# Optimization experiments

Measured on AMD Instinct MI355X. Metric: run time of the kernel, lower is better.

Reference implementation:

```python
import jax, jax.numpy as jnp
import numpy as np

D_MODEL = 1024
HEADS = 16
SCALE = float(np.sqrt(D_MODEL / HEADS))  # sqrt(d_k) = sqrt(64) = 8


def setup_inputs() -> dict:
    key = jax.random.key(0)
    ks = jax.random.split(key, 5)
    B, S, D = 4, 2048, D_MODEL
    q = jax.random.normal(ks[0], (B, S, D), dtype=jnp.float32)
    init = 0.02
    wq = jax.random.normal(ks[1], (D, D), dtype=jnp.float32) * init
    wk = jax.random.normal(ks[2], (D, D), dtype=jnp.float32) * init
    wv = jax.random.normal(ks[3], (D, D), dtype=jnp.float32) * init
    wo = jax.random.normal(ks[4], (D, D), dtype=jnp.float32) * init
    return {"q": q, "wq": wq, "wk": wk, "wv": wv, "wo": wo}


def reference(q, wq, wk, wv, wo):
    # Faithful to the source: NO head split is ever performed.
    B, S, D = q.shape
    # nn.Linear convention: y = x @ W.T, weight is [out, in]
    Q = jnp.einsum('bsd,ed->bse', q, wq)
    K = jnp.einsum('bsd,ed->bse', q, wk)
    V = jnp.einsum('bsd,ed->bse', q, wv)
    scores = jnp.einsum('bqe,bke->bqk', Q, K) / SCALE  # [B, S, S]
    attn = jax.nn.softmax(scores, axis=-1)
    out = jnp.einsum('bqk,bke->bqe', attn, V)  # [B, S, D]
    # Source bug reproduced: transpose(1,2).contiguous().view(B, S, -1)
    # => reshape the [B, D, S] contiguous buffer back to [B, S, D].
    out = jnp.transpose(out, (0, 2, 1)).reshape(B, S, D)
    return jnp.einsum('bsd,ed->bse', out, wo)
```

## Files before the change

kernel.cpp:

```cpp
#include <hip/hip_runtime.h>
#include <hip/hip_bf16.h>
#include <stdint.h>

typedef __bf16 bf16;
typedef __attribute__((ext_vector_type(8))) __bf16 bf16x8;
typedef __attribute__((ext_vector_type(4))) float f32x4;
typedef __attribute__((ext_vector_type(8))) unsigned short u16x8;

#define LDS_U32 __attribute__((address_space(3))) uint32_t
#define GLB_U32 const __attribute__((address_space(1))) uint32_t
#define GLOAD16(g, l) __builtin_amdgcn_global_load_lds((GLB_U32*)(g), (LDS_U32*)(l), 16, 0, 0)

#define DSR(dst, addr, OFFLIT) \
  asm volatile("ds_read_b128 %0, %1 offset:" OFFLIT : "=v"(dst) : "v"(addr))

#define WAIT_LGKM0() asm volatile("s_waitcnt lgkmcnt(0)")
#define WAIT_LGKM4() asm volatile("s_waitcnt lgkmcnt(4)")
#define WAIT_VMN(n)  asm volatile("s_waitcnt vmcnt(" #n ")")
#define SB()         __builtin_amdgcn_sched_barrier(0)

__global__ __launch_bounds__(256) void cvt_all(const float* __restrict__ q,
                                               const float* __restrict__ wq,
                                               const float* __restrict__ wk,
                                               const float* __restrict__ wv,
                                               const float* __restrict__ wo,
                                               bf16* __restrict__ qb,
                                               bf16* __restrict__ W3,
                                               bf16* __restrict__ wob) {
  const int b = blockIdx.x;
  const float* src;
  bf16* dst;
  int within;
  if (b < 2048) { src = q; dst = qb; within = b; }
  else {
    const int seg = (b - 2048) >> 8;
    within = (b - 2048) & 255;
    if (seg == 0)      { src = wq; dst = W3; }
    else if (seg == 1) { src = wk; dst = W3 + 1048576; }
    else if (seg == 2) { src = wv; dst = W3 + 2097152; }
    else               { src = wo; dst = wob; }
  }
  const int off = within * 1024;
#pragma unroll
  for (int it = 0; it < 4; ++it) {
    const int j = off + it * 256 + threadIdx.x;
    float4 v = reinterpret_cast<const float4*>(src)[j];
    ushort4 o;
    o.x = __builtin_bit_cast(unsigned short, (bf16)v.x);
    o.y = __builtin_bit_cast(unsigned short, (bf16)v.y);
    o.z = __builtin_bit_cast(unsigned short, (bf16)v.z);
    o.w = __builtin_bit_cast(unsigned short, (bf16)v.w);
    reinterpret_cast<ushort4*>(dst)[j] = o;
  }
}

template <int EPI, int WN>
__global__ __launch_bounds__(512, 2) void g256(const bf16* __restrict__ A,
                                               const bf16* __restrict__ Bm,
                                               void* __restrict__ Cp,
                                               int K, float alpha,
                                               long sA, long sB, long sC, int ldc,
                                               int CW, int CH) {
  constexpr int BN = WN * 64;
  constexpr uint32_t PARB = 32768u + WN * 8192u;
  __shared__ bf16 smem_[PARB];
  const long z = blockIdx.z;
  const int t = threadIdx.x;
  const int l = t & 63;
  const int w = t >> 6;
  const int wr = (w >> 2) * 128;
  const int wc = (w & 3) * (WN * 16);
  const int NT = K >> 6;

  int bx, by;
  {
    const int gx = (int)gridDim.x;
    const int gy = (int)gridDim.y;
    const int nxy = gx * gy;
    const int f = (int)blockIdx.y * gx + (int)blockIdx.x;
    const int cgx = (CW > 0) ? gx / CW : 0;
    if ((nxy & 7) == 0 && CW > 0 && CH > 0 && gx % CW == 0 && gy % CH == 0 &&
        cgx * (gy / CH) == 8) {
      const int xcd = f & 7;
      const int i = f >> 3;
      const int cx = xcd % cgx;
      const int cy = xcd / cgx;
      bx = cx * CW + (i % CW);
      by = cy * CH + (i / CW);
    } else if ((nxy & 7) == 0) {
      const int qq = nxy >> 3;
      const int wg = (f & 7) * qq + (f >> 3);
      bx = wg % gx;
      by = wg / gx;
    } else {
      bx = (int)blockIdx.x;
      by = (int)blockIdx.y;
    }
  }

  const bf16* Ab = A + z * sA + (long)(by * 256) * K;
  const bf16* Bb = Bm + z * sB + (long)(bx * BN) * K;

  uint32_t loc = (uint32_t)t * 16u;
  uint32_t g0 = loc ^ (((loc >> 9) & 1u) << 5);
  const int r0 = (int)(((g0 >> 10) >> 1) * 16 + ((g0 >> 6) & 15));
  const int c0 = (int)(((g0 >> 10) & 1) * 32 + ((g0 & 63) >> 1));

  uint32_t lo_ = (uint32_t)((l & 15) * 64 + (l >> 4) * 16);
  const uint32_t lane_off = lo_ ^ (((lo_ >> 9) & 1u) << 5);
  const uint32_t aRegion = (uint32_t)(wr >> 7) * 16384u;
  const uint32_t smem_base = (uint32_t)(size_t)&smem_[0];
  const uint32_t aBase = smem_base + aRegion + lane_off;

  uint32_t bA[WN];
#pragma unroll
  for (int n = 0; n < WN; ++n) {
    const uint32_t row = (uint32_t)(wc + n * 16);
    bA[n] = smem_base + 32768u + (row >> 6) * 8192u + ((row & 63u) >> 4) * 2048u + lane_off;
  }

  auto STAGE1 = [&](const bf16* mat, int unit, int tile, uint32_t isB) {
    uint32_t dst = (uint32_t)(tile & 1) * PARB + isB + (uint32_t)unit * 8192u + (uint32_t)t * 16u;
    const bf16* src = mat + (long)(unit * 64 + r0) * K + tile * 64 + c0;
    GLOAD16(src, smem_ + (dst >> 1));
  };

  f32x4 acc[8][WN] = {};

  STAGE1(Ab, 0, 0, 0u); STAGE1(Ab, 1, 0, 0u); STAGE1(Ab, 2, 0, 0u); STAGE1(Ab, 3, 0, 0u);
#pragma unroll
  for (int u = 0; u < WN; ++u) STAGE1(Bb, u, 0, 32768u);
  SB();
  WAIT_VMN(0);
  __builtin_amdgcn_s_barrier();

#define MFMAQ(Q, S)                                                                  \
  _Pragma("unroll") for (int mi = 0; mi < 2; ++mi)                                   \
  _Pragma("unroll") for (int n = 0; n < WN; ++n)                                     \
  _Pragma("unroll") for (int kk = 0; kk < 2; ++kk)                                   \
    acc[(Q) * 2 + mi][n] = __builtin_amdgcn_mfma_f32_16x16x32_bf16(                  \
        __builtin_bit_cast(bf16x8, aF[S][mi][kk]), __builtin_bit_cast(bf16x8, bF[n][kk]), \
        acc[(Q) * 2 + mi][n], 0, 0, 0);

  for (int T = 0; T < NT; ++T) {
    const uint32_t pb = (uint32_t)(T & 1) * PARB;
    const uint32_t aA = aBase + pb;
    f32x4 bF[WN][2];
    f32x4 aF[2][2][2];

    if (T + 1 < NT) {
#pragma unroll
      for (int u = 0; u < WN; ++u) STAGE1(Bb, u, T + 1, 32768u);
      STAGE1(Ab, 0, T + 1, 0u); STAGE1(Ab, 2, T + 1, 0u);
    }

#pragma unroll
    for (int n = 0; n < WN; ++n) {
      DSR(bF[n][0], bA[n] + pb, "0");
      DSR(bF[n][1], bA[n] + pb, "1024");
    }
    DSR(aF[0][0][0], aA, "0");    DSR(aF[0][0][1], aA, "1024");
    DSR(aF[0][1][0], aA, "2048"); DSR(aF[0][1][1], aA, "3072");
    DSR(aF[1][0][0], aA, "4096"); DSR(aF[1][0][1], aA, "5120");
    DSR(aF[1][1][0], aA, "6144"); DSR(aF[1][1][1], aA, "7168");
    WAIT_LGKM4();
    SB();
    __builtin_amdgcn_s_setprio(1);
    MFMAQ(0, 0)
    __builtin_amdgcn_s_setprio(0);
    WAIT_LGKM0();
    SB();
    __builtin_amdgcn_s_setprio(1);
    MFMAQ(1, 1)
    __builtin_amdgcn_s_setprio(0);

    if (T + 1 < NT) { STAGE1(Ab, 1, T + 1, 0u); STAGE1(Ab, 3, T + 1, 0u); }

    SB();
    if (T + 1 < NT) {
      if constexpr (WN == 2) { WAIT_VMN(6); } else { WAIT_VMN(8); }
    } else {
      WAIT_VMN(0);
    }
    __builtin_amdgcn_s_barrier();

    DSR(aF[0][0][0], aA, "8192");  DSR(aF[0][0][1], aA, "9216");
    DSR(aF[0][1][0], aA, "10240"); DSR(aF[0][1][1], aA, "11264");
    DSR(aF[1][0][0], aA, "12288"); DSR(aF[1][0][1], aA, "13312");
    DSR(aF[1][1][0], aA, "14336"); DSR(aF[1][1][1], aA, "15360");
    WAIT_LGKM4();
    SB();
    __builtin_amdgcn_s_setprio(1);
    MFMAQ(2, 0)
    __builtin_amdgcn_s_setprio(0);
    WAIT_LGKM0();
    SB();
    __builtin_amdgcn_s_setprio(1);
    MFMAQ(3, 1)
    __builtin_amdgcn_s_setprio(0);

    SB();
    if (T + 1 < NT) { WAIT_VMN(2); } else { WAIT_VMN(0); }
    __builtin_amdgcn_s_barrier();
  }
#undef MFMAQ

  if constexpr (EPI == 4) {
    constexpr int STR = 264;
#pragma unroll
    for (int m = 0; m < 8; ++m)
#pragma unroll
      for (int n = 0; n < WN; ++n) {
        const int e = wc + n * 16 + (l & 15);
        const int s = wr + (l >> 4) * 4 + m * 16;
        ushort4 pk;
        pk.x = __builtin_bit_cast(unsigned short, (bf16)(acc[m][n][0] * alpha));
        pk.y = __builtin_bit_cast(unsigned short, (bf16)(acc[m][n][1] * alpha));
        pk.z = __builtin_bit_cast(unsigned short, (bf16)(acc[m][n][2] * alpha));
        pk.w = __builtin_bit_cast(unsigned short, (bf16)(acc[m][n][3] * alpha));
        *reinterpret_cast<ushort4*>(&smem_[e * STR + s]) = pk;
      }
    __syncthreads();
    bf16* Vt = (bf16*)Cp;
    const int bq = by >> 3;
    const int sbase = (by & 7) * 256;
    const int e0 = t >> 2;
#pragma unroll
    for (int it = 0; it < 8; ++it) {
      const int c = (t & 3) + it * 4;
      uint4 v = *reinterpret_cast<const uint4*>(&smem_[e0 * STR + c * 8]);
      *reinterpret_cast<uint4*>(
          &Vt[(long)bq * 2097152 + (long)(bx * BN + e0) * 2048 + sbase + c * 8]) = v;
    }
    return;
  }

  if constexpr (EPI == 6) {
    {
      const int orow0 = by * 256 + wr + (l >> 4) * 4;
      const int ocol0 = bx * 256 + wc + (l & 15);
      bf16* Qb = (bf16*)Cp;
      bf16* Kb = Qb + 8388608;
#pragma unroll
      for (int m = 0; m < 8; ++m)
#pragma unroll
        for (int n = 0; n < WN; ++n)
#pragma unroll
          for (int i = 0; i < 4; ++i) {
            const long r = orow0 + m * 16 + i;
            const long c = ocol0 + n * 16;
            const float v = acc[m][n][i];
            if (c < 1024) Qb[r * 1024 + c] = (bf16)v;
            else Kb[r * 1024 + (c - 1024)] = (bf16)v;
          }
    }
    const bf16* Bv = Bm + 2 * 1048576 + (long)(bx * 128) * K;
    uint32_t bA2[2];
#pragma unroll
    for (int n = 0; n < 2; ++n) {
      const uint32_t row = (uint32_t)((w & 3) * 32 + n * 16);
      bA2[n] = smem_base + 32768u + (row >> 6) * 8192u + ((row & 63u) >> 4) * 2048u + lane_off;
    }
#pragma unroll
    for (int m = 0; m < 8; ++m)
#pragma unroll
      for (int n = 0; n < 2; ++n) acc[m][n] = f32x4{0.f, 0.f, 0.f, 0.f};

    __builtin_amdgcn_s_barrier();
    STAGE1(Ab, 0, 0, 0u); STAGE1(Ab, 1, 0, 0u); STAGE1(Ab, 2, 0, 0u); STAGE1(Ab, 3, 0, 0u);
    STAGE1(Bv, 0, 0, 32768u); STAGE1(Bv, 1, 0, 32768u);
    SB();
    WAIT_VMN(0);
    __builtin_amdgcn_s_barrier();

#define MFMAQ2(Q, S)                                                                 \
    _Pragma("unroll") for (int mi = 0; mi < 2; ++mi)                                 \
    _Pragma("unroll") for (int n = 0; n < 2; ++n)                                    \
    _Pragma("unroll") for (int kk = 0; kk < 2; ++kk)                                 \
      acc[(Q) * 2 + mi][n] = __builtin_amdgcn_mfma_f32_16x16x32_bf16(                \
          __builtin_bit_cast(bf16x8, aF[S][mi][kk]), __builtin_bit_cast(bf16x8, bF2[n][kk]), \
          acc[(Q) * 2 + mi][n], 0, 0, 0);

    for (int T = 0; T < NT; ++T) {
      const uint32_t pb = (uint32_t)(T & 1) * PARB;
      const uint32_t aA = aBase + pb;
      f32x4 bF2[2][2];
      f32x4 aF[2][2][2];
      if (T + 1 < NT) {
        STAGE1(Ab, 0, T + 1, 0u); STAGE1(Ab, 1, T + 1, 0u);
        STAGE1(Ab, 2, T + 1, 0u); STAGE1(Ab, 3, T + 1, 0u);
        STAGE1(Bv, 0, T + 1, 32768u); STAGE1(Bv, 1, T + 1, 32768u);
      }
      DSR(bF2[0][0], bA2[0] + pb, "0"); DSR(bF2[0][1], bA2[0] + pb, "1024");
      DSR(bF2[1][0], bA2[1] + pb, "0"); DSR(bF2[1][1], bA2[1] + pb, "1024");
      DSR(aF[0][0][0], aA, "0");    DSR(aF[0][0][1], aA, "1024");
      DSR(aF[0][1][0], aA, "2048"); DSR(aF[0][1][1], aA, "3072");
      DSR(aF[1][0][0], aA, "4096"); DSR(aF[1][0][1], aA, "5120");
      DSR(aF[1][1][0], aA, "6144"); DSR(aF[1][1][1], aA, "7168");
      WAIT_LGKM4();
      SB();
      __builtin_amdgcn_s_setprio(1);
      MFMAQ2(0, 0)
      __builtin_amdgcn_s_setprio(0);
      WAIT_LGKM0();
      SB();
      __builtin_amdgcn_s_setprio(1);
      MFMAQ2(1, 1)
      __builtin_amdgcn_s_setprio(0);
      DSR(aF[0][0][0], aA, "8192");  DSR(aF[0][0][1], aA, "9216");
      DSR(aF[0][1][0], aA, "10240"); DSR(aF[0][1][1], aA, "11264");
      DSR(aF[1][0][0], aA, "12288"); DSR(aF[1][0][1], aA, "13312");
      DSR(aF[1][1][0], aA, "14336"); DSR(aF[1][1][1], aA, "15360");
      WAIT_LGKM4();
      SB();
      __builtin_amdgcn_s_setprio(1);
      MFMAQ2(2, 0)
      __builtin_amdgcn_s_setprio(0);
      WAIT_LGKM0();
      SB();
      __builtin_amdgcn_s_setprio(1);
      MFMAQ2(3, 1)
      __builtin_amdgcn_s_setprio(0);
      SB();
      if (T + 1 < NT) { WAIT_VMN(0); } else { WAIT_VMN(0); }
      __builtin_amdgcn_s_barrier();
    }
#undef MFMAQ2

    {
      constexpr int STR = 264;
#pragma unroll
      for (int m = 0; m < 8; ++m)
#pragma unroll
        for (int n = 0; n < 2; ++n) {
          const int e = (w & 3) * 32 + n * 16 + (l & 15);
          const int s = wr + (l >> 4) * 4 + m * 16;
          ushort4 pk;
          pk.x = __builtin_bit_cast(unsigned short, (bf16)acc[m][n][0]);
          pk.y = __builtin_bit_cast(unsigned short, (bf16)acc[m][n][1]);
          pk.z = __builtin_bit_cast(unsigned short, (bf16)acc[m][n][2]);
          pk.w = __builtin_bit_cast(unsigned short, (bf16)acc[m][n][3]);
          *reinterpret_cast<ushort4*>(&smem_[e * STR + s]) = pk;
        }
      __syncthreads();
      bf16* Vt = (bf16*)Cp + 2 * 8388608;
      const int bq = by >> 3;
      const int sbase = (by & 7) * 256;
      const int e0 = t >> 2;
#pragma unroll
      for (int it = 0; it < 8; ++it) {
        const int c = (t & 3) + it * 4;
        uint4 v = *reinterpret_cast<const uint4*>(&smem_[e0 * STR + c * 8]);
        *reinterpret_cast<uint4*>(
            &Vt[(long)bq * 2097152 + (long)(bx * 128 + e0) * 2048 + sbase + c * 8]) = v;
      }
    }
    return;
  }

  const int orow0 = by * 256 + wr + (l >> 4) * 4;
  const int ocol0 = bx * BN + wc + (l & 15);
#pragma unroll
  for (int m = 0; m < 8; ++m)
#pragma unroll
    for (int n = 0; n < WN; ++n)
#pragma unroll
      for (int i = 0; i < 4; ++i) {
        const long r = orow0 + m * 16 + i;
        const long c = ocol0 + n * 16;
        const float v = acc[m][n][i] * alpha;
        if constexpr (EPI == 0) {
          ((bf16*)Cp)[z * sC + r * ldc + c] = (bf16)v;
        } else if constexpr (EPI == 2) {
          ((float*)Cp)[r * ldc + c] = v;
        }
      }
}

__global__ __launch_bounds__(256) void softmax_rows(bf16* __restrict__ P) {
  const long row = blockIdx.x;
  bf16* p = P + row * 2048;
  const int t = threadIdx.x;
  const int lane = t & 63;
  const int wave = t >> 6;

  u16x8 raw = *reinterpret_cast<const u16x8*>(p + t * 8);
  float v[8];
#pragma unroll
  for (int j = 0; j < 8; ++j) {
    uint32_t bits = ((uint32_t)raw[j]) << 16;
    v[j] = __builtin_bit_cast(float, bits);
  }
  float m = v[0];
#pragma unroll
  for (int j = 1; j < 8; ++j) m = fmaxf(m, v[j]);
#pragma unroll
  for (int off = 32; off > 0; off >>= 1) m = fmaxf(m, __shfl_xor(m, off, 64));
  __shared__ float redm[4];
  __shared__ float reds[4];
  if (lane == 0) redm[wave] = m;
  __syncthreads();
  m = fmaxf(fmaxf(redm[0], redm[1]), fmaxf(redm[2], redm[3]));

  float s = 0.f;
#pragma unroll
  for (int j = 0; j < 8; ++j) {
    v[j] = __expf(v[j] - m);
    s += v[j];
  }
#pragma unroll
  for (int off = 32; off > 0; off >>= 1) s += __shfl_xor(s, off, 64);
  if (lane == 0) reds[wave] = s;
  __syncthreads();
  s = reds[0] + reds[1] + reds[2] + reds[3];
  const float inv = 1.f / s;

  u16x8 o;
#pragma unroll
  for (int j = 0; j < 8; ++j) o[j] = __builtin_bit_cast(unsigned short, (bf16)(v[j] * inv));
  *reinterpret_cast<u16x8*>(p + t * 8) = o;
}

extern "C" void kernel_launch(void* const* d_in, const int* in_sizes, int n_in,
                              void* d_out, int out_size, void* d_ws, size_t ws_size,
                              hipStream_t stream) {
  const float* q = (const float*)d_in[0];
  const float* wq = (const float*)d_in[1];
  const float* wk = (const float*)d_in[2];
  const float* wv = (const float*)d_in[3];
  const float* wo = (const float*)d_in[4];
  float* out = (float*)d_out;

  constexpr int B = 4, S = 2048, D = 1024;
  constexpr long SD = (long)S * D;
  constexpr long SS = (long)S * S;
  constexpr long DD = (long)D * D;

  bf16* wsb = (bf16*)d_ws;
  bf16* qb = wsb;
  bf16* W3 = qb + B * SD;
  bf16* wob = W3 + 3 * DD;
  bf16* Qb = wob + DD;
  bf16* Kb = Qb + B * SD;
  bf16* Vt = Kb + B * SD;
  bf16* P = Vt + B * SD;
  bf16* X = P + B * SS;

  cvt_all<<<3072, 256, 0, stream>>>(q, wq, wk, wv, wo, qb, W3, wob);

  g256<6, 4><<<dim3(8, 32, 1), 512, 0, stream>>>(qb, W3, Qb, D, 1.f, 0, 0, 0, 0, 4, 8);
  g256<0, 4><<<dim3(8, 8, B), 512, 0, stream>>>(Qb, Kb, P, D, 0.125f, SD, SD, SS, S, 4, 2);
  softmax_rows<<<B * S, 256, 0, stream>>>(P);
  g256<0, 2><<<dim3(16, 4, B), 512, 0, stream>>>(Vt, P, X, S, 1.f, SD, SS, SD, S, 4, 2);
  g256<2, 2><<<dim3(8, 32, 1), 512, 0, stream>>>(X, wob, out, D, 1.f, 0, 0, 0, D, 4, 8);
}
```

Before: 181.2 us.

## Claim GEMM tiles dynamically per XCD via atomic counters with work stealing

Replaces the static blockIdx-to-tile mapping with a dynamic claim. Each workgroup reads its hardware XCC ID and atomically takes the next tile from that XCD's chunk, falling back to other XCDs' chunks once its own is exhausted. The goal is to keep each XCD's tiles in its own L2 even though the dispatch order does not follow blockIdx, and to balance load across XCDs. The counters are zeroed in the conversion kernel, and the change adds an atomic plus a block barrier at the start of each GEMM block. It also pads the LDS transpose stride from 264 to 268 to reduce bank conflicts in the epilogue and simplifies a redundant wait.

```diff
diff --git a/kernel.cpp b/kernel.cpp
--- a/kernel.cpp
+++ b/kernel.cpp
@@ -26,8 +26,10 @@
                                                const float* __restrict__ wo,
                                                bf16* __restrict__ qb,
                                                bf16* __restrict__ W3,
-                                               bf16* __restrict__ wob) {
+                                               bf16* __restrict__ wob,
+                                               int* __restrict__ cnts) {
   const int b = blockIdx.x;
+  if (b == 0 && cnts && threadIdx.x < 96) cnts[threadIdx.x] = 0;
   const float* src;
   bf16* dst;
   int within;
@@ -60,10 +62,12 @@
                                                void* __restrict__ Cp,
                                                int K, float alpha,
                                                long sA, long sB, long sC, int ldc,
-                                               int CW, int CH) {
+                                               int CW, int CH,
+                                               int* __restrict__ cnt) {
   constexpr int BN = WN * 64;
   constexpr uint32_t PARB = 32768u + WN * 8192u;
   __shared__ bf16 smem_[PARB];
+  __shared__ int claim_s;
   const long z = blockIdx.z;
   const int t = threadIdx.x;
   const int l = t & 63;
@@ -77,10 +81,34 @@
     const int gx = (int)gridDim.x;
     const int gy = (int)gridDim.y;
     const int nxy = gx * gy;
-    const int f = (int)blockIdx.y * gx + (int)blockIdx.x;
     const int cgx = (CW > 0) ? gx / CW : 0;
-    if ((nxy & 7) == 0 && CW > 0 && CH > 0 && gx % CW == 0 && gy % CH == 0 &&
-        cgx * (gy / CH) == 8) {
+    const bool chunk_ok = (nxy & 7) == 0 && CW > 0 && CH > 0 && gx % CW == 0 &&
+                          gy % CH == 0 && cgx * (gy / CH) == 8;
+    if (cnt && chunk_ok) {
+      const int csz = nxy >> 3;
+      if (t == 0) {
+        uint32_t xcc;
+        asm volatile("s_getreg_b32 %0, hwreg(HW_REG_XCC_ID)" : "=s"(xcc));
+        const int xcd = (int)(xcc & 7);
+        int tile = 0;
+#pragma unroll 1
+        for (int probe = 0; probe < 8; ++probe) {
+          const int x = (xcd + probe) & 7;
+          const int s = atomicAdd(&cnt[(int)z * 8 + x], 1);
+          if (s < csz) { tile = x * csz + s; break; }
+        }
+        claim_s = tile;
+      }
+      __syncthreads();
+      const int tile = claim_s;
+      const int c = tile / csz;
+      const int i2 = tile % csz;
+      const int cx = c % cgx;
+      const int cy = c / cgx;
+      bx = cx * CW + (i2 % CW);
+      by = cy * CH + (i2 / CW);
+    } else if (chunk_ok) {
+      const int f = (int)blockIdx.y * gx + (int)blockIdx.x;
       const int xcd = f & 7;
       const int i = f >> 3;
       const int cx = xcd % cgx;
@@ -88,6 +116,7 @@
       bx = cx * CW + (i % CW);
       by = cy * CH + (i / CW);
     } else if ((nxy & 7) == 0) {
+      const int f = (int)blockIdx.y * gx + (int)blockIdx.x;
       const int qq = nxy >> 3;
       const int wg = (f & 7) * qq + (f >> 3);
       bx = wg % gx;
@@ -206,7 +235,7 @@
 #undef MFMAQ
 
   if constexpr (EPI == 4) {
-    constexpr int STR = 264;
+    constexpr int STR = 268;
 #pragma unroll
     for (int m = 0; m < 8; ++m)
 #pragma unroll
@@ -322,13 +351,13 @@
       MFMAQ2(3, 1)
       __builtin_amdgcn_s_setprio(0);
       SB();
-      if (T + 1 < NT) { WAIT_VMN(0); } else { WAIT_VMN(0); }
+      WAIT_VMN(0);
       __builtin_amdgcn_s_barrier();
     }
 #undef MFMAQ2
 
     {
-      constexpr int STR = 264;
+      constexpr int STR = 268;
 #pragma unroll
       for (int m = 0; m < 8; ++m)
 #pragma unroll
@@ -446,11 +475,18 @@
   bf16* P = Vt + B * SD;
   bf16* X = P + B * SS;
 
-  cvt_all<<<3072, 256, 0, stream>>>(q, wq, wk, wv, wo, qb, W3, wob);
-
-  g256<6, 4><<<dim3(8, 32, 1), 512, 0, stream>>>(qb, W3, Qb, D, 1.f, 0, 0, 0, 0, 4, 8);
-  g256<0, 4><<<dim3(8, 8, B), 512, 0, stream>>>(Qb, Kb, P, D, 0.125f, SD, SD, SS, S, 4, 2);
+  const size_t used_b = (size_t)(X + B * SD - wsb) * sizeof(bf16);
+  int* cnts = (ws_size >= used_b + 512) ? (int*)((char*)d_ws + used_b) : nullptr;
+  int* cQKV = cnts;
+  int* cSC  = cnts ? cnts + 8 : nullptr;
+  int* cPV  = cnts ? cnts + 40 : nullptr;
+  int* cOP  = cnts ? cnts + 72 : nullptr;
+
+  cvt_all<<<3072, 256, 0, stream>>>(q, wq, wk, wv, wo, qb, W3, wob, cnts);
+
+  g256<6, 4><<<dim3(8, 32, 1), 512, 0, stream>>>(qb, W3, Qb, D, 1.f, 0, 0, 0, 0, 4, 8, cQKV);
+  g256<0, 4><<<dim3(8, 8, B), 512, 0, stream>>>(Qb, Kb, P, D, 0.125f, SD, SD, SS, S, 4, 2, cSC);
   softmax_rows<<<B * S, 256, 0, stream>>>(P);
-  g256<0, 2><<<dim3(16, 4, B), 512, 0, stream>>>(Vt, P, X, S, 1.f, SD, SS, SD, S, 4, 2);
-  g256<2, 2><<<dim3(8, 32, 1), 512, 0, stream>>>(X, wob, out, D, 1.f, 0, 0, 0, D, 4, 8);
+  g256<0, 2><<<dim3(16, 4, B), 512, 0, stream>>>(Vt, P, X, S, 1.f, SD, SS, SD, S, 4, 2, cPV);
+  g256<2, 2><<<dim3(8, 32, 1), 512, 0, stream>>>(X, wob, out, D, 1.f, 0, 0, 0, D, 4, 8, cOP);
 }
```

Result: no change. 184.6 us (+1.9%).
